# Optimization experiments

Hardware: AMD Instinct MI355X
Metric: run time of the kernel (lower is better)

Reference implementation:

```python
import jax, jax.numpy as jnp
import numpy as np

B, S, HID, NH = 4, 2048, 1024, 16
DH = HID // NH  # 64
SCALE = 1.0 / float(np.sqrt(DH))


def _linear_params(key, scale=0.02):
    kw, kb = jax.random.split(key)
    W = jax.random.normal(kw, (HID, HID), dtype=jnp.float32) * scale
    b = jax.random.normal(kb, (HID,), dtype=jnp.float32) * scale
    return W, b


def setup_inputs() -> dict:
    key = jax.random.key(0)
    ks = jax.random.split(key, 9)
    x = jax.random.normal(ks[0], (B, S, HID), dtype=jnp.float32)
    reasoning_mask = jax.random.uniform(ks[1], (B, S, 1, 1), dtype=jnp.float32)
    Wq, bq = _linear_params(ks[2])
    Wk, bk = _linear_params(ks[3])
    Wv, bv = _linear_params(ks[4])
    Wqr, bqr = _linear_params(ks[5])
    Wkr, bkr = _linear_params(ks[6])
    Wo, bo = _linear_params(ks[7])
    return {"x": x, "reasoning_mask": reasoning_mask,
            "Wq": Wq, "bq": bq, "Wk": Wk, "bk": bk, "Wv": Wv, "bv": bv,
            "Wqr": Wqr, "bqr": bqr, "Wkr": Wkr, "bkr": bkr, "Wo": Wo, "bo": bo}


def reference(x, reasoning_mask, Wq, bq, Wk, bk, Wv, bv, Wqr, bqr, Wkr, bkr, Wo, bo):
    # Projections: x @ W + b, then view (B, S, NH, DH)
    def proj(W, b):
        return (jnp.einsum('bsh,hd->bsd', x, W) + b).reshape(B, S, NH, DH)

    q = proj(Wq, bq)
    k = proj(Wk, bk)
    v = proj(Wv, bv)
    q_r = proj(Wqr, bqr)
    k_r = proj(Wkr, bkr)

    # Reasoning-gated blend of standard and reasoning projections
    q = q * (1.0 - reasoning_mask) + q_r * reasoning_mask
    k = k * (1.0 - reasoning_mask) + k_r * reasoning_mask

    # Faithful to source: matmul over the LAST two dims of (B,S,NH,DH),
    # i.e. per-token attention ACROSS HEADS -> scores shape (B,S,NH,NH)
    scores = jnp.einsum('bshd,bsed->bshe', q, k) * SCALE
    attn = jax.nn.softmax(scores, axis=-1)  # dropout is identity at eval
    out = jnp.einsum('bshe,bsed->bshd', attn, v)  # (B,S,NH,DH)

    # Faithful transpose(1,2) + contiguous view to (B, S, HID)
    out = jnp.transpose(out, (0, 2, 1, 3)).reshape(B, -1, HID)
    return jnp.einsum('bsh,hd->bsd', out, Wo) + bo
```

## Files before the change

kernel.cpp:

```cpp
#include <hip/hip_runtime.h>
#include <hip/hip_bf16.h>


typedef __attribute__((ext_vector_type(8))) short short8;
typedef __attribute__((ext_vector_type(4))) short short4v;
typedef __attribute__((ext_vector_type(4))) float f32x4;

#define HID 1024
#define NTOK 8192
#define WT_ELEMS (1024 * 1024)

__device__ __forceinline__ short f2bs(float f) {
  __hip_bfloat16 h = __float2bfloat16(f);
  return *reinterpret_cast<short*>(&h);
}
__device__ __forceinline__ float bs2f(short s) {
  __hip_bfloat16 h;
  *reinterpret_cast<short*>(&h) = s;
  return __bfloat162float(h);
}
__device__ __forceinline__ void gload16(const void* g, void* l) {
  __builtin_amdgcn_global_load_lds(
      (const __attribute__((address_space(1))) void*)g,
      (__attribute__((address_space(3))) void*)l, 16, 0, 0);
}

#define BAR() asm volatile("s_barrier" ::: "memory")
#define VMWAIT(N) asm volatile("s_waitcnt vmcnt(" #N ")" ::: "memory")
#define LGKM0 do { asm volatile("s_waitcnt lgkmcnt(0)" ::: "memory"); \
                   __builtin_amdgcn_sched_barrier(0); } while (0)
#define SCB __builtin_amdgcn_sched_barrier(0)
#define PRIO1 __builtin_amdgcn_s_setprio(1)
#define PRIO0 __builtin_amdgcn_s_setprio(0)
#define MFMA16x16 __builtin_amdgcn_mfma_f32_16x16x32_bf16

__global__ __launch_bounds__(256) void prep_kernel(
    const float* __restrict__ W0, const float* __restrict__ W1,
    const float* __restrict__ W2, const float* __restrict__ W3,
    const float* __restrict__ W4, const float* __restrict__ W5,
    const float* __restrict__ X, short* __restrict__ WT, short* __restrict__ XB)
{
  __shared__ short sT[64][68];
  const int bid = blockIdx.x, tid = threadIdx.x;
  if (bid < 1536) {
    const int z = bid >> 8, rem = bid & 255;
    const float* W = z == 0 ? W0 : z == 1 ? W1 : z == 2 ? W2 : z == 3 ? W3
                   : z == 4 ? W4 : W5;
    short* OUT = WT + (size_t)z * WT_ELEMS;
    const int k0 = (rem & 15) * 64, n0 = (rem >> 4) * 64;
    #pragma unroll
    for (int i = 0; i < 4; i++) {
      const int li = tid + i * 256;
      const int kr = li >> 4, c4 = (li & 15) << 2;
      const f32x4 wv = *reinterpret_cast<const f32x4*>(&W[(size_t)(k0 + kr) * HID + n0 + c4]);
      short4v s4;
      #pragma unroll
      for (int j = 0; j < 4; j++) s4[j] = f2bs(wv[j]);
      *reinterpret_cast<short4v*>(&sT[kr][c4]) = s4;
    }
    __syncthreads();
    #pragma unroll
    for (int i = 0; i < 4; i++) {
      const int li = tid + i * 256;
      const int nr = li >> 4, k4 = (li & 15) << 2;
      short4v o;
      #pragma unroll
      for (int j = 0; j < 4; j++) o[j] = sT[k4 + j][nr];
      const int kcol = (k0 + k4) ^ ((nr & 7) << 3);
      *reinterpret_cast<short4v*>(&OUT[(size_t)(n0 + nr) * HID + kcol]) = o;
    }
  } else {
    const int gid = (bid - 1536) * 256 + tid;
    const int row = gid >> 7, kc = (gid & 127) << 3;
    const f32x4 a = *reinterpret_cast<const f32x4*>(&X[(size_t)row * HID + kc]);
    const f32x4 b = *reinterpret_cast<const f32x4*>(&X[(size_t)row * HID + kc + 4]);
    short8 s;
    #pragma unroll
    for (int j = 0; j < 4; j++) { s[j] = f2bs(a[j]); s[4 + j] = f2bs(b[j]); }
    const int phys = (kc & ~63) | ((kc & 63) ^ ((row & 7) << 3));
    *reinterpret_cast<short8*>(&XB[(size_t)row * HID + phys]) = s;
  }
}

__global__ __launch_bounds__(512, 2) void gated8_kernel(
    const short* __restrict__ XB, const short* __restrict__ WTbase,
    const float* __restrict__ bq, const float* __restrict__ bqr,
    const float* __restrict__ bk, const float* __restrict__ bkr,
    const float* __restrict__ MASK,
    __hip_bfloat16* __restrict__ qg, __hip_bfloat16* __restrict__ kg)
{
  __shared__ short lA[2][256][64];
  __shared__ short lB1[2][128][64];
  __shared__ short lB2[2][128][64];

  const int z = blockIdx.z;
  const short* W1T = WTbase + (size_t)(2 * z) * WT_ELEMS;
  const short* W2T = W1T + WT_ELEMS;
  const float* B1b = z ? bk : bq;
  const float* B2b = z ? bkr : bqr;
  __hip_bfloat16* OUT = z ? kg : qg;

  const int m0 = blockIdx.x * 256, n0 = blockIdx.y * 128;
  const int tid = threadIdx.x, lane = tid & 63, w = tid >> 6;
  const int wr = (w >> 1) * 64, wc = (w & 1) * 64;
  const int lrow = lane & 15, lkhi = (lane >> 4) << 3;
  const int swz = (lrow & 7) << 3;
  const int srow = lane >> 3, scol = (lane & 7) << 3;

  f32x4 acc1[4][4] = {}, acc2[4][4] = {};
  short8 bf1k[4], bf2k[4];
  short8 af0, af1, af2, af3;

  auto stA2 = [&](int slot, int kt, int i0) {
    const int k0 = kt * 64;
    #pragma unroll
    for (int i = 0; i < 2; i++) {
      const int chunk = w * 4 + i0 + i;
      gload16(&XB[(size_t)(m0 + chunk * 8 + srow) * HID + k0 + scol],
              &lA[slot][chunk * 8][0]);
    }
  };
  auto stB1s = [&](int slot, int kt) {
    const int k0 = kt * 64;
    #pragma unroll
    for (int i = 0; i < 2; i++) {
      const int chunk = w * 2 + i;
      gload16(&W1T[(size_t)(n0 + chunk * 8 + srow) * HID + k0 + scol],
              &lB1[slot][chunk * 8][0]);
    }
  };
  auto stB2s = [&](int slot, int kt) {
    const int k0 = kt * 64;
    #pragma unroll
    for (int i = 0; i < 2; i++) {
      const int chunk = w * 2 + i;
      gload16(&W2T[(size_t)(n0 + chunk * 8 + srow) * HID + k0 + scol],
              &lB2[slot][chunk * 8][0]);
    }
  };
  auto rdA = [&](int s, int m, int kk) -> short8 {
    const int lk = (kk * 32 + lkhi) ^ swz;
    return *reinterpret_cast<const short8*>(&lA[s][wr + m * 16 + lrow][lk]);
  };

#define RDB1(S, KK)                                                                   \
  _Pragma("unroll")                                                                   \
  for (int n = 0; n < 4; n++) {                                                       \
    const int lk = ((KK) * 32 + lkhi) ^ swz;                                          \
    bf1k[n] = *reinterpret_cast<const short8*>(&lB1[S][wc + n * 16 + lrow][lk]);      \
  }
#define RDB2(S, KK)                                                                   \
  _Pragma("unroll")                                                                   \
  for (int n = 0; n < 4; n++) {                                                       \
    const int lk = ((KK) * 32 + lkhi) ^ swz;                                          \
    bf2k[n] = *reinterpret_cast<const short8*>(&lB2[S][wc + n * 16 + lrow][lk]);      \
  }
#define MM16A                                                             \
  _Pragma("unroll")                                                       \
  for (int n = 0; n < 4; n++) {                                           \
    acc1[0][n] = MFMA16x16(af0, bf1k[n], acc1[0][n], 0, 0, 0);            \
    acc1[1][n] = MFMA16x16(af1, bf1k[n], acc1[1][n], 0, 0, 0);            \
    acc1[2][n] = MFMA16x16(af2, bf1k[n], acc1[2][n], 0, 0, 0);            \
    acc1[3][n] = MFMA16x16(af3, bf1k[n], acc1[3][n], 0, 0, 0);            \
  }
#define MM16B                                                             \
  _Pragma("unroll")                                                       \
  for (int n = 0; n < 4; n++) {                                           \
    acc2[0][n] = MFMA16x16(af0, bf2k[n], acc2[0][n], 0, 0, 0);            \
    acc2[1][n] = MFMA16x16(af1, bf2k[n], acc2[1][n], 0, 0, 0);            \
    acc2[2][n] = MFMA16x16(af2, bf2k[n], acc2[2][n], 0, 0, 0);            \
    acc2[3][n] = MFMA16x16(af3, bf2k[n], acc2[3][n], 0, 0, 0);            \
  }
#define GTILE(S, SN, TS)                                                 \
                         \
  af0 = rdA(S, 0, 0); af1 = rdA(S, 1, 0);                                \
  af2 = rdA(S, 2, 0); af3 = rdA(S, 3, 0);                                \
  RDB1(S, 0);                                                            \
  stA2(SN, TS, 0); stA2(SN, TS, 2);                                      \
  BAR(); LGKM0;                                                          \
  PRIO1; MM16A PRIO0; SCB;                                               \
  BAR();                                                                 \
                         \
  RDB2(S, 0);                                                            \
  stB1s(SN, TS); stB2s(SN, TS);                                          \
  BAR(); LGKM0;                                                          \
  PRIO1; MM16B PRIO0; SCB;                                               \
  BAR();                                                                 \
                                          \
  af0 = rdA(S, 0, 1); af1 = rdA(S, 1, 1);                                \
  af2 = rdA(S, 2, 1); af3 = rdA(S, 3, 1);                                \
  RDB1(S, 1);                                                            \
  BAR(); LGKM0;                                                          \
  PRIO1; MM16A PRIO0; SCB;                                               \
  BAR();                                                                 \
                       \
  RDB2(S, 1);                                                            \
  BAR(); LGKM0;                                                          \
  PRIO1; MM16B PRIO0; SCB;                                               \
  VMWAIT(0);                                                             \
  BAR();

  stA2(0, 0, 0); stA2(0, 0, 2); stB1s(0, 0); stB2s(0, 0);
  VMWAIT(0);
  BAR();

  #pragma unroll 1
  for (int i = 0; i < 8; i++) {
    const int tb = 2 * i + 1;
    const int tn = (i < 7) ? 2 * i + 2 : 15;
    GTILE(0, 1, tb)
    GTILE(1, 0, tn)
  }
#undef GTILE
#undef MM16A
#undef MM16B
#undef RDB1
#undef RDB2

  #pragma unroll
  for (int m = 0; m < 4; m++) {
    const int rbase = m0 + wr + m * 16 + ((lane >> 4) << 2);
    #pragma unroll
    for (int n = 0; n < 4; n++) {
      const int col = n0 + wc + n * 16 + lrow;
      const float bias1 = B1b[col];
      const float bias2 = B2b[col];
      #pragma unroll
      for (int r = 0; r < 4; r++) {
        const int row = rbase + r;
        const float mk = MASK[row];
        const float val = (acc1[m][n][r] + bias1) * (1.f - mk) +
                          (acc2[m][n][r] + bias2) * mk;
        OUT[(size_t)row * HID + col] = __float2bfloat16(val);
      }
    }
  }
}

template<bool OUTF32>
__global__ __launch_bounds__(512, 2) void plain8_kernel(
    const short* __restrict__ A, const short* __restrict__ WT,
    const float* __restrict__ BIAS, void* __restrict__ OUTv)
{
  __shared__ short lA[2][256][64];
  __shared__ short lB[2][128][64];

  const int m0 = blockIdx.x * 256, n0 = blockIdx.y * 128;
  const int tid = threadIdx.x, lane = tid & 63, w = tid >> 6;
  const int wr = (w >> 1) * 64, wc = (w & 1) * 64;
  const int lrow = lane & 15, lkhi = (lane >> 4) << 3;
  const int swz = (lrow & 7) << 3;
  const int srow = lane >> 3, scol = (lane & 7) << 3;

  f32x4 acc[4][4] = {};
  short8 paf[4], pbf[4];

  auto stTrip = [&](int slot, int kt, int t) {
    const int k0 = kt * 64;
    if (t == 0) {
      #pragma unroll
      for (int i = 0; i < 3; i++) {
        const int chunk = w * 4 + i;
        gload16(&A[(size_t)(m0 + chunk * 8 + srow) * HID + k0 + scol],
                &lA[slot][chunk * 8][0]);
      }
    } else {
      const int chunk = w * 4 + 3;
      gload16(&A[(size_t)(m0 + chunk * 8 + srow) * HID + k0 + scol],
              &lA[slot][chunk * 8][0]);
      #pragma unroll
      for (int i = 0; i < 2; i++) {
        const int bchunk = w * 2 + i;
        gload16(&WT[(size_t)(n0 + bchunk * 8 + srow) * HID + k0 + scol],
                &lB[slot][bchunk * 8][0]);
      }
    }
  };

#define RDP(S, KK)                                                                    \
  _Pragma("unroll")                                                                   \
  for (int m = 0; m < 4; m++) {                                                       \
    const int lk = ((KK) * 32 + lkhi) ^ swz;                                          \
    paf[m] = *reinterpret_cast<const short8*>(&lA[S][wr + m * 16 + lrow][lk]);        \
    pbf[m] = *reinterpret_cast<const short8*>(&lB[S][wc + m * 16 + lrow][lk]);        \
  }
#define PMM16                                                                         \
  _Pragma("unroll")                                                                   \
  for (int m = 0; m < 4; m++)                                                         \
    _Pragma("unroll")                                                                 \
    for (int n = 0; n < 4; n++)                                                       \
      acc[m][n] = MFMA16x16(paf[m], pbf[n], acc[m][n], 0, 0, 0);
#define PTILE(S, SN, TS)        \
                        \
  RDP(S, 0)                     \
  stTrip(SN, TS, 0);            \
  BAR(); LGKM0;                 \
  PRIO1; PMM16 PRIO0; SCB;      \
  BAR();                        \
                        \
  RDP(S, 1)                     \
  stTrip(SN, TS, 1);            \
  BAR(); LGKM0;                 \
  PRIO1; PMM16 PRIO0; SCB;      \
  VMWAIT(0);                    \
  BAR();

  stTrip(0, 0, 0); stTrip(0, 0, 1);
  VMWAIT(0);
  BAR();

  #pragma unroll 1
  for (int i = 0; i < 8; i++) {
    const int tb = 2 * i + 1;
    const int tn = (i < 7) ? 2 * i + 2 : 15;
    PTILE(0, 1, tb)
    PTILE(1, 0, tn)
  }
#undef PTILE
#undef PMM16
#undef RDP

  #pragma unroll
  for (int m = 0; m < 4; m++) {
    const int rbase = m0 + wr + m * 16 + ((lane >> 4) << 2);
    #pragma unroll
    for (int n = 0; n < 4; n++) {
      const int col = n0 + wc + n * 16 + lrow;
      const float bias = BIAS[col];
      #pragma unroll
      for (int r = 0; r < 4; r++) {
        const float val = acc[m][n][r] + bias;
        const size_t oidx = (size_t)(rbase + r) * HID + col;
        if (OUTF32) ((float*)OUTv)[oidx] = val;
        else ((__hip_bfloat16*)OUTv)[oidx] = __float2bfloat16(val);
      }
    }
  }
}

__global__ __launch_bounds__(256) void attn_kernel(
    const __hip_bfloat16* __restrict__ Q, const __hip_bfloat16* __restrict__ K,
    const __hip_bfloat16* __restrict__ V, __hip_bfloat16* __restrict__ O)
{
  const int t = blockIdx.x;
  const int b = t >> 11, s = t & 2047;
  __shared__ float sQ[16][68], sK[16][68], sV[16][68];
  __shared__ float sA[16][17];
  const int tid = threadIdx.x;
  const size_t tb = (size_t)t * HID;

  {
    const int h = tid >> 4, d0 = (tid & 15) << 2;
    const int o = (h << 6) + d0;
    const short4v qv = *reinterpret_cast<const short4v*>(&((const short*)Q)[tb + o]);
    const short4v kv = *reinterpret_cast<const short4v*>(&((const short*)K)[tb + o]);
    const short4v vv = *reinterpret_cast<const short4v*>(&((const short*)V)[tb + o]);
    #pragma unroll
    for (int j = 0; j < 4; j++) {
      sQ[h][d0 + j] = bs2f(qv[j]);
      sK[h][d0 + j] = bs2f(kv[j]);
      sV[h][d0 + j] = bs2f(vv[j]);
    }
  }
  __syncthreads();

  const int h = tid >> 4, e = tid & 15;
  float sc = 0.f;
  #pragma unroll
  for (int d = 0; d < 64; d++) sc += sQ[h][d] * sK[e][d];
  sc *= 0.125f;

  float mx = sc;
  mx = fmaxf(mx, __shfl_xor(mx, 1));
  mx = fmaxf(mx, __shfl_xor(mx, 2));
  mx = fmaxf(mx, __shfl_xor(mx, 4));
  mx = fmaxf(mx, __shfl_xor(mx, 8));
  const float p = __expf(sc - mx);
  float sm = p;
  sm += __shfl_xor(sm, 1);
  sm += __shfl_xor(sm, 2);
  sm += __shfl_xor(sm, 4);
  sm += __shfl_xor(sm, 8);
  sA[h][e] = p / sm;
  __syncthreads();

  const int row7 = (s >> 4) & 7;
  const size_t ob = ((size_t)b * 2048 + (s >> 4)) * HID + ((size_t)(s & 15) << 6);
  {
    const int hh = tid >> 4, d4 = (tid & 15) << 2;
    f32x4 o = {0.f, 0.f, 0.f, 0.f};
    #pragma unroll
    for (int e2 = 0; e2 < 16; e2++) {
      const float a = sA[hh][e2];
      #pragma unroll
      for (int j = 0; j < 4; j++) o[j] += a * sV[e2][d4 + j];
    }
    short4v ov;
    #pragma unroll
    for (int j = 0; j < 4; j++) ov[j] = f2bs(o[j]);
    *reinterpret_cast<short4v*>(
        &((short*)O)[ob + (size_t)hh * 128 * HID + (d4 ^ (row7 << 3))]) = ov;
  }
}

extern "C" void kernel_launch(void* const* d_in, const int* in_sizes, int n_in,
                              void* d_out, int out_size, void* d_ws, size_t ws_size,
                              hipStream_t stream) {
  (void)in_sizes; (void)n_in; (void)out_size; (void)ws_size;
  const float* x   = (const float*)d_in[0];
  const float* rm  = (const float*)d_in[1];
  const float* Wq  = (const float*)d_in[2];
  const float* bq  = (const float*)d_in[3];
  const float* Wk  = (const float*)d_in[4];
  const float* bk  = (const float*)d_in[5];
  const float* Wv  = (const float*)d_in[6];
  const float* bv  = (const float*)d_in[7];
  const float* Wqr = (const float*)d_in[8];
  const float* bqr = (const float*)d_in[9];
  const float* Wkr = (const float*)d_in[10];
  const float* bkr = (const float*)d_in[11];
  const float* Wo  = (const float*)d_in[12];
  const float* bo  = (const float*)d_in[13];

  char* ws = (char*)d_ws;
  short* wt = (short*)ws;
  __hip_bfloat16* qg = (__hip_bfloat16*)(ws + 12u * 1024 * 1024);
  __hip_bfloat16* vv = (__hip_bfloat16*)(ws + 28u * 1024 * 1024);
  __hip_bfloat16* ar = (__hip_bfloat16*)(ws + 44u * 1024 * 1024);
  short* xb = (short*)d_out;
  __hip_bfloat16* kg = (__hip_bfloat16*)((char*)d_out + 16u * 1024 * 1024);

  prep_kernel<<<dim3(5632), 256, 0, stream>>>(Wq, Wqr, Wk, Wkr, Wv, Wo, x, wt, xb);
  gated8_kernel<<<dim3(32, 8, 2), 512, 0, stream>>>(xb, wt, bq, bqr, bk, bkr, rm, qg, kg);
  plain8_kernel<false><<<dim3(32, 8), 512, 0, stream>>>(xb, wt + (size_t)4 * WT_ELEMS, bv, vv);
  attn_kernel<<<dim3(NTOK), 256, 0, stream>>>(qg, kg, vv, ar);
  plain8_kernel<true><<<dim3(32, 8), 512, 0, stream>>>((const short*)ar,
                                                       wt + (size_t)5 * WT_ELEMS, bo, d_out);
}
```

Measured before the change: 152.3 us.

## Remap GEMM blocks for XCD locality and deepen load pipelining

Both GEMM kernels now launch a 1D grid and remap the block index so blocks that share output tiles are grouped on the same XCD, aiming to improve L2 reuse on MI355X's chiplet layout. The gated kernel relaxes vmcnt waits so the next tile's global loads stay in flight across stages. The plain kernel moves from double to triple-buffered LDS, prefetching two tiles ahead, to hide global-load latency. Triple buffering raises LDS use per block, which can lower occupancy, and the partial vmcnt counts must match the actual number of issued loads to stay correct.

```diff
diff --git a/kernel.cpp b/kernel.cpp
--- a/kernel.cpp
+++ b/kernel.cpp
@@ -93,14 +93,18 @@
   __shared__ short lB1[2][128][64];
   __shared__ short lB2[2][128][64];
 
-  const int z = blockIdx.z;
+  const int d = blockIdx.x;
+  const int li = (d & 7) * 64 + (d >> 3);
+  const int bx = li & 31, byz = li >> 5;
+  const int by = byz & 7, z = byz >> 3;
+
   const short* W1T = WTbase + (size_t)(2 * z) * WT_ELEMS;
   const short* W2T = W1T + WT_ELEMS;
   const float* B1b = z ? bk : bq;
   const float* B2b = z ? bkr : bqr;
   __hip_bfloat16* OUT = z ? kg : qg;
 
-  const int m0 = blockIdx.x * 256, n0 = blockIdx.y * 128;
+  const int m0 = bx * 256, n0 = by * 128;
   const int tid = threadIdx.x, lane = tid & 63, w = tid >> 6;
   const int wr = (w >> 1) * 64, wc = (w & 1) * 64;
   const int lrow = lane & 15, lkhi = (lane >> 4) << 3;
@@ -172,45 +176,46 @@
     acc2[3][n] = MFMA16x16(af3, bf2k[n], acc2[3][n], 0, 0, 0);            \
   }
 #define GTILE(S, SN, TS)                                                 \
-                         \
+                                                                 \
   af0 = rdA(S, 0, 0); af1 = rdA(S, 1, 0);                                \
   af2 = rdA(S, 2, 0); af3 = rdA(S, 3, 0);                                \
   RDB1(S, 0);                                                            \
   stA2(SN, TS, 0); stA2(SN, TS, 2);                                      \
   BAR(); LGKM0;                                                          \
   PRIO1; MM16A PRIO0; SCB;                                               \
+  VMWAIT(4);                                                             \
   BAR();                                                                 \
-                         \
+                                                                 \
   RDB2(S, 0);                                                            \
   stB1s(SN, TS); stB2s(SN, TS);                                          \
   BAR(); LGKM0;                                                          \
   PRIO1; MM16B PRIO0; SCB;                                               \
   BAR();                                                                 \
-                                          \
+                                                                 \
   af0 = rdA(S, 0, 1); af1 = rdA(S, 1, 1);                                \
   af2 = rdA(S, 2, 1); af3 = rdA(S, 3, 1);                                \
   RDB1(S, 1);                                                            \
   BAR(); LGKM0;                                                          \
   PRIO1; MM16A PRIO0; SCB;                                               \
   BAR();                                                                 \
-                       \
+                                                                 \
   RDB2(S, 1);                                                            \
   BAR(); LGKM0;                                                          \
   PRIO1; MM16B PRIO0; SCB;                                               \
-  VMWAIT(0);                                                             \
+  VMWAIT(2);                                                             \
   BAR();
 
   stA2(0, 0, 0); stA2(0, 0, 2); stB1s(0, 0); stB2s(0, 0);
+  VMWAIT(2);
+  BAR();
+
+  #pragma unroll 1
+  for (int i = 0; i < 16; i++) {
+    const int S = i & 1, SN = S ^ 1;
+    const int TS = (i < 15) ? i + 1 : 15;
+    GTILE(S, SN, TS)
+  }
   VMWAIT(0);
-  BAR();
-
-  #pragma unroll 1
-  for (int i = 0; i < 8; i++) {
-    const int tb = 2 * i + 1;
-    const int tn = (i < 7) ? 2 * i + 2 : 15;
-    GTILE(0, 1, tb)
-    GTILE(1, 0, tn)
-  }
 #undef GTILE
 #undef MM16A
 #undef MM16B
@@ -242,10 +247,14 @@
     const short* __restrict__ A, const short* __restrict__ WT,
     const float* __restrict__ BIAS, void* __restrict__ OUTv)
 {
-  __shared__ short lA[2][256][64];
-  __shared__ short lB[2][128][64];
-
-  const int m0 = blockIdx.x * 256, n0 = blockIdx.y * 128;
+  __shared__ short lA[3][256][64];
+  __shared__ short lB[3][128][64];
+
+  const int d = blockIdx.x;
+  const int li = (d & 7) * 32 + (d >> 3);
+  const int bx = li & 31, by = li >> 5;
+
+  const int m0 = bx * 256, n0 = by * 128;
   const int tid = threadIdx.x, lane = tid & 63, w = tid >> 6;
   const int wr = (w >> 1) * 64, wc = (w & 1) * 64;
   const int lrow = lane & 15, lkhi = (lane >> 4) << 3;
@@ -290,33 +299,31 @@
     _Pragma("unroll")                                                                 \
     for (int n = 0; n < 4; n++)                                                       \
       acc[m][n] = MFMA16x16(paf[m], pbf[n], acc[m][n], 0, 0, 0);
-#define PTILE(S, SN, TS)        \
-                        \
-  RDP(S, 0)                     \
-  stTrip(SN, TS, 0);            \
-  BAR(); LGKM0;                 \
-  PRIO1; PMM16 PRIO0; SCB;      \
-  BAR();                        \
-                        \
-  RDP(S, 1)                     \
-  stTrip(SN, TS, 1);            \
-  BAR(); LGKM0;                 \
-  PRIO1; PMM16 PRIO0; SCB;      \
-  VMWAIT(0);                    \
+
+  stTrip(0, 0, 0); stTrip(0, 0, 1);
+  stTrip(1, 1, 0); stTrip(1, 1, 1);
+  VMWAIT(6);
   BAR();
 
-  stTrip(0, 0, 0); stTrip(0, 0, 1);
+  int s = 0, s2 = 2;
+  #pragma unroll 1
+  for (int t = 0; t < 16; t++) {
+    const int TS = (t < 14) ? t + 2 : 15;
+    RDP(s, 0)
+    stTrip(s2, TS, 0);
+    BAR(); LGKM0;
+    PRIO1; PMM16 PRIO0; SCB;
+    BAR();
+    RDP(s, 1)
+    stTrip(s2, TS, 1);
+    BAR(); LGKM0;
+    PRIO1; PMM16 PRIO0; SCB;
+    VMWAIT(6);
+    BAR();
+    s = (s == 2) ? 0 : s + 1;
+    s2 = (s2 == 2) ? 0 : s2 + 1;
+  }
   VMWAIT(0);
-  BAR();
-
-  #pragma unroll 1
-  for (int i = 0; i < 8; i++) {
-    const int tb = 2 * i + 1;
-    const int tn = (i < 7) ? 2 * i + 2 : 15;
-    PTILE(0, 1, tb)
-    PTILE(1, 0, tn)
-  }
-#undef PTILE
 #undef PMM16
 #undef RDP
 
@@ -367,7 +374,7 @@
   const int h = tid >> 4, e = tid & 15;
   float sc = 0.f;
   #pragma unroll
-  for (int d = 0; d < 64; d++) sc += sQ[h][d] * sK[e][d];
+  for (int dd = 0; dd < 64; dd++) sc += sQ[h][dd] * sK[e][dd];
   sc *= 0.125f;
 
   float mx = sc;
@@ -431,9 +438,9 @@
   __hip_bfloat16* kg = (__hip_bfloat16*)((char*)d_out + 16u * 1024 * 1024);
 
   prep_kernel<<<dim3(5632), 256, 0, stream>>>(Wq, Wqr, Wk, Wkr, Wv, Wo, x, wt, xb);
-  gated8_kernel<<<dim3(32, 8, 2), 512, 0, stream>>>(xb, wt, bq, bqr, bk, bkr, rm, qg, kg);
-  plain8_kernel<false><<<dim3(32, 8), 512, 0, stream>>>(xb, wt + (size_t)4 * WT_ELEMS, bv, vv);
+  gated8_kernel<<<dim3(512), 512, 0, stream>>>(xb, wt, bq, bqr, bk, bkr, rm, qg, kg);
+  plain8_kernel<false><<<dim3(256), 512, 0, stream>>>(xb, wt + (size_t)4 * WT_ELEMS, bv, vv);
   attn_kernel<<<dim3(NTOK), 256, 0, stream>>>(qg, kg, vv, ar);
-  plain8_kernel<true><<<dim3(32, 8), 512, 0, stream>>>((const short*)ar,
-                                                       wt + (size_t)5 * WT_ELEMS, bo, d_out);
-}
+  plain8_kernel<true><<<dim3(256), 512, 0, stream>>>((const short*)ar,
+                                                     wt + (size_t)5 * WT_ELEMS, bo, d_out);
+}
```

Measured after the change: 167.3 us. 9.8% more time.
